# Optimization experiments

Hardware: AMD Instinct MI355X
Metric: run time of the kernel (lower is better)

The kernel has to match this reference:

```python
import jax, jax.numpy as jnp
import numpy as np

N = 50000      # atoms
E = 800000     # edges (flat neighbor list)
ELEM = 64      # elem_fea_len
NBR = 64       # nbr_fea_len
EPS = 1e-5


def _bn(x, gamma, beta):
    # BatchNorm1d in training mode: biased batch stats over dim 0
    mean = jnp.mean(x, axis=0)
    var = jnp.mean(jnp.square(x - mean), axis=0)
    return (x - mean) * jax.lax.rsqrt(var + EPS) * gamma + beta


def setup_inputs() -> dict:
    key = jax.random.key(0)
    ks = jax.random.split(key, 8)
    atom_in_fea = jax.random.normal(ks[0], (N, ELEM), dtype=jnp.float32)
    nbr_fea = jax.random.normal(ks[1], (E, NBR), dtype=jnp.float32)
    self_fea_idx = jnp.sort(jax.random.randint(ks[2], (E,), 0, N))
    nbr_fea_idx = jax.random.randint(ks[3], (E,), 0, N)
    d_in = 2 * ELEM + NBR
    d_out = 2 * ELEM
    W = jax.random.normal(ks[4], (d_in, d_out), dtype=jnp.float32) / np.sqrt(d_in)
    b = jax.random.normal(ks[5], (d_out,), dtype=jnp.float32) * 0.01
    bn1_gamma = jnp.ones((d_out,), jnp.float32)
    bn1_beta = jnp.zeros((d_out,), jnp.float32)
    bn2_gamma = jnp.ones((ELEM,), jnp.float32)
    bn2_beta = jnp.zeros((ELEM,), jnp.float32)
    return {
        "atom_in_fea": atom_in_fea, "nbr_fea": nbr_fea,
        "self_fea_idx": self_fea_idx, "nbr_fea_idx": nbr_fea_idx,
        "W": W, "b": b,
        "bn1_gamma": bn1_gamma, "bn1_beta": bn1_beta,
        "bn2_gamma": bn2_gamma, "bn2_beta": bn2_beta,
    }


def reference(atom_in_fea, nbr_fea, self_fea_idx, nbr_fea_idx,
              W, b, bn1_gamma, bn1_beta, bn2_gamma, bn2_beta):
    n_atoms = atom_in_fea.shape[0]
    # gather endpoint features: (E, ELEM) each
    atom_self = atom_in_fea[self_fea_idx]
    atom_nbr = atom_in_fea[nbr_fea_idx]
    total = jnp.concatenate([atom_self, atom_nbr, nbr_fea], axis=1)  # (E, 2*ELEM+NBR)
    total = total @ W + b                                            # (E, 2*ELEM)
    total = _bn(total, bn1_gamma, bn1_beta)
    filter_fea, core_fea = jnp.split(total, 2, axis=1)
    nbr_msg = jax.nn.sigmoid(filter_fea) * jax.nn.softplus(core_fea)  # (E, ELEM)
    nbr_sumed = jax.ops.segment_sum(nbr_msg, self_fea_idx, num_segments=n_atoms)
    nbr_sumed = _bn(nbr_sumed, bn2_gamma, bn2_beta)
    return jax.nn.softplus(atom_in_fea + nbr_sumed)
```

## Files before the change

kernel.cpp:

```cpp
#include <hip/hip_runtime.h>

typedef unsigned short ushort_t;
typedef __attribute__((ext_vector_type(8))) short short8;
typedef __attribute__((ext_vector_type(4))) float f32x4;

constexpr int N_ATOMS = 50000;
constexpr int N_EDGES = 800000;
constexpr int ELEM    = 64;
constexpr int D_IN    = 192;
constexpr int D_OUT   = 128;
constexpr float EPS   = 1e-5f;

constexpr int TILE_M = 64;
constexpr int NREP   = 16;

constexpr size_t OFF_NS   = 0;
constexpr size_t OFF_ABF  = OFF_NS   + (size_t)N_ATOMS * ELEM * 4;
constexpr size_t OFF_WT   = OFF_ABF  + (size_t)N_ATOMS * ELEM * 2;
constexpr size_t OFF_BN1  = OFF_WT   + (size_t)D_OUT * D_IN * 2;
constexpr size_t OFF_SC1  = OFF_BN1  + NREP * 256 * 4;
constexpr size_t OFF_BN2  = OFF_SC1  + 256 * 4;
constexpr size_t OFF_SC2  = OFF_BN2  + NREP * 128 * 4;

__device__ __forceinline__ ushort_t f32_to_bf16(float f) {
    unsigned int u = __float_as_uint(f);
    u = (u + 0x7fffu + ((u >> 16) & 1u)) >> 16;
    return (ushort_t)u;
}
__device__ __forceinline__ float bf16_to_f32(ushort_t h) {
    return __uint_as_float(((unsigned int)h) << 16);
}
__device__ __forceinline__ float softplus_f(float x) {
    return fmaxf(x, 0.f) + __logf(1.f + __expf(-fabsf(x)));
}

__global__ void prep_init_kernel(const float* __restrict__ atom, const float* __restrict__ W,
                                 ushort_t* __restrict__ abf, ushort_t* __restrict__ Wt,
                                 float* __restrict__ ns,
                                 float* __restrict__ bn1r, float* __restrict__ bn2r) {
    int i = blockIdx.x * blockDim.x + threadIdx.x;
    if (i < N_ATOMS * ELEM) { abf[i] = f32_to_bf16(atom[i]); ns[i] = 0.f; }
    if (i < D_IN * D_OUT) {
        int k = i >> 7, n = i & 127;
        Wt[n * D_IN + k] = f32_to_bf16(W[i]);
    }
    if (i < NREP * 256) bn1r[i] = 0.f;
    if (i < NREP * 128) bn2r[i] = 0.f;
}

__device__ __forceinline__ void stage_A(ushort_t (*As)[200],
                                        const ushort_t* __restrict__ abf,
                                        const float* __restrict__ nbrf,
                                        const int* __restrict__ sidx,
                                        const int* __restrict__ nidx,
                                        int e0, int tid) {
    #pragma unroll
    for (int ch = 0; ch < 2; ++ch) {
        const int* __restrict__ idx = ch ? nidx : sidx;
        #pragma unroll
        for (int i = 0; i < 2; ++i) {
            int r = (tid >> 3) + 32 * i;
            int h = tid & 7;
            const uint4* src = (const uint4*)(abf + (size_t)idx[e0 + r] * 64);
            *(uint4*)&As[r][ch * 64 + h * 8] = src[h];
        }
    }
    #pragma unroll
    for (int i = 0; i < 4; ++i) {
        int r  = (tid >> 4) + 16 * i;
        int c4 = tid & 15;
        float4 v = *(const float4*)(nbrf + (size_t)(e0 + r) * 64 + c4 * 4);
        ushort4 pk;
        pk.x = f32_to_bf16(v.x); pk.y = f32_to_bf16(v.y);
        pk.z = f32_to_bf16(v.z); pk.w = f32_to_bf16(v.w);
        *(ushort4*)&As[r][128 + c4 * 4] = pk;
    }
}

__global__ __launch_bounds__(256) void stats_kernel(
    const ushort_t* __restrict__ abf, const float* __restrict__ nbrf,
    const int* __restrict__ sidx, const int* __restrict__ nidx,
    const ushort_t* __restrict__ Wt, const float* __restrict__ bias,
    float* __restrict__ bn1r)
{
    __shared__ __align__(16) ushort_t As[64][200];
    const int tid = threadIdx.x;
    const int e0  = blockIdx.x * TILE_M;

    stage_A(As, abf, nbrf, sidx, nidx, e0, tid);

    const int wave = tid >> 6, lane = tid & 63;
    const int m16 = lane & 15, quad = lane >> 4;

    short8 bfrag[2][6];
    #pragma unroll
    for (int nt = 0; nt < 2; ++nt) {
        const ushort_t* bp = Wt + (size_t)(wave * 32 + nt * 16 + m16) * D_IN + quad * 8;
        #pragma unroll
        for (int ks = 0; ks < 6; ++ks) bfrag[nt][ks] = *(const short8*)(bp + ks * 32);
    }
    __syncthreads();

    f32x4 acc[4][2];
    #pragma unroll
    for (int mt = 0; mt < 4; ++mt)
        #pragma unroll
        for (int nt = 0; nt < 2; ++nt) acc[mt][nt] = (f32x4){0.f, 0.f, 0.f, 0.f};

    #pragma unroll
    for (int ks = 0; ks < 6; ++ks) {
        int ko = ks * 32 + quad * 8;
        #pragma unroll
        for (int mt = 0; mt < 4; ++mt) {
            short8 a = *(const short8*)&As[mt * 16 + m16][ko];
            acc[mt][0] = __builtin_amdgcn_mfma_f32_16x16x32_bf16(a, bfrag[0][ks], acc[mt][0], 0, 0, 0);
            acc[mt][1] = __builtin_amdgcn_mfma_f32_16x16x32_bf16(a, bfrag[1][ks], acc[mt][1], 0, 0, 0);
        }
    }

    float* rep = bn1r + (size_t)(blockIdx.x & (NREP - 1)) * 256;
    #pragma unroll
    for (int nt = 0; nt < 2; ++nt) {
        int c = wave * 32 + nt * 16 + m16;
        float b = bias[c];
        float s = 0.f, q = 0.f;
        #pragma unroll
        for (int mt = 0; mt < 4; ++mt)
            #pragma unroll
            for (int r = 0; r < 4; ++r) {
                float v = acc[mt][nt][r] + b;
                s += v; q += v * v;
            }
        s += __shfl_xor(s, 16); s += __shfl_xor(s, 32);
        q += __shfl_xor(q, 16); q += __shfl_xor(q, 32);
        if (quad == 0) {
            atomicAdd(&rep[c], s);
            atomicAdd(&rep[128 + c], q);
        }
    }
}

__global__ void bn1_finalize(const float* __restrict__ bn1r,
                             const float* __restrict__ g1, const float* __restrict__ b1,
                             float* __restrict__ sc) {
    int c = threadIdx.x;
    float s = 0.f, q = 0.f;
    #pragma unroll
    for (int r = 0; r < NREP; ++r) { s += bn1r[r * 256 + c]; q += bn1r[r * 256 + 128 + c]; }
    float mean = s * (1.f / N_EDGES);
    float var  = q * (1.f / N_EDGES) - mean * mean;
    float scale = g1[c] * rsqrtf(var + EPS);
    sc[c] = scale;
    sc[128 + c] = b1[c] - mean * scale;
}

__global__ __launch_bounds__(256) void msg_kernel(
    const ushort_t* __restrict__ abf, const float* __restrict__ nbrf,
    const int* __restrict__ sidx, const int* __restrict__ nidx,
    const ushort_t* __restrict__ Wt, const float* __restrict__ bias,
    const float* __restrict__ sc, float* __restrict__ ns)
{
    __shared__ __align__(16) char smem[25600];
    ushort_t (*As)[200] = (ushort_t(*)[200])smem;
    float    (*Ms)[68]  = (float(*)[68])smem;
    __shared__ int ss[64];

    const int tid = threadIdx.x;
    const int e0  = blockIdx.x * TILE_M;

    stage_A(As, abf, nbrf, sidx, nidx, e0, tid);
    if (tid < 64) ss[tid] = sidx[e0 + tid];

    const int wave = tid >> 6, lane = tid & 63;
    const int m16 = lane & 15, quad = lane >> 4;
    const int cf = wave * 16 + m16;
    const int cc = 64 + cf;

    short8 bfrag[2][6];
    {
        const ushort_t* bp0 = Wt + (size_t)cf * D_IN + quad * 8;
        const ushort_t* bp1 = Wt + (size_t)cc * D_IN + quad * 8;
        #pragma unroll
        for (int ks = 0; ks < 6; ++ks) {
            bfrag[0][ks] = *(const short8*)(bp0 + ks * 32);
            bfrag[1][ks] = *(const short8*)(bp1 + ks * 32);
        }
    }
    __syncthreads();

    f32x4 acc[4][2];
    #pragma unroll
    for (int mt = 0; mt < 4; ++mt)
        #pragma unroll
        for (int nt = 0; nt < 2; ++nt) acc[mt][nt] = (f32x4){0.f, 0.f, 0.f, 0.f};

    #pragma unroll
    for (int ks = 0; ks < 6; ++ks) {
        int ko = ks * 32 + quad * 8;
        #pragma unroll
        for (int mt = 0; mt < 4; ++mt) {
            short8 a = *(const short8*)&As[mt * 16 + m16][ko];
            acc[mt][0] = __builtin_amdgcn_mfma_f32_16x16x32_bf16(a, bfrag[0][ks], acc[mt][0], 0, 0, 0);
            acc[mt][1] = __builtin_amdgcn_mfma_f32_16x16x32_bf16(a, bfrag[1][ks], acc[mt][1], 0, 0, 0);
        }
    }
    __syncthreads();

    {
        float bf_ = bias[cf], bc_ = bias[cc];
        float scf = sc[cf], shf = sc[128 + cf];
        float scc = sc[cc], shc = sc[128 + cc];
        #pragma unroll
        for (int mt = 0; mt < 4; ++mt) {
            int row = mt * 16 + quad * 4;
            #pragma unroll
            for (int r = 0; r < 4; ++r) {
                float yf = fmaf(acc[mt][0][r] + bf_, scf, shf);
                float yc = fmaf(acc[mt][1][r] + bc_, scc, shc);
                Ms[row + r][cf] = softplus_f(yc) / (1.f + __expf(-yf));
            }
        }
    }
    __syncthreads();

    {
        int v = tid >> 6, c = tid & 63;
        int base = v * 16;
        int cur = ss[base];
        float a = 0.f;
        #pragma unroll
        for (int r = 0; r < 16; ++r) {
            int s = ss[base + r];
            if (s != cur) { atomicAdd(&ns[(size_t)cur * 64 + c], a); cur = s; a = 0.f; }
            a += Ms[base + r][c];
        }
        atomicAdd(&ns[(size_t)cur * 64 + c], a);
    }
}

__global__ __launch_bounds__(256) void bn2_stats_kernel(
    const float* __restrict__ ns, float* __restrict__ bn2r)
{
    int c = threadIdx.x & 63;
    float s = 0.f, q = 0.f;
    for (int a = blockIdx.x * 4 + (threadIdx.x >> 6); a < N_ATOMS; a += 4096) {
        float v = ns[a * ELEM + c];
        s += v; q += v * v;
    }
    float* rep = bn2r + (size_t)(blockIdx.x & (NREP - 1)) * 128;
    atomicAdd(&rep[c], s);
    atomicAdd(&rep[64 + c], q);
}

__global__ void bn2_finalize(const float* __restrict__ bn2r,
                             const float* __restrict__ g2, const float* __restrict__ b2,
                             float* __restrict__ sc2) {
    int c = threadIdx.x;
    float s = 0.f, q = 0.f;
    #pragma unroll
    for (int r = 0; r < NREP; ++r) { s += bn2r[r * 128 + c]; q += bn2r[r * 128 + 64 + c]; }
    float mean = s * (1.f / N_ATOMS);
    float var  = q * (1.f / N_ATOMS) - mean * mean;
    float scale = g2[c] * rsqrtf(var + EPS);
    sc2[c] = scale;
    sc2[64 + c] = b2[c] - mean * scale;
}

__global__ void final_kernel(const float* __restrict__ atom, const float* __restrict__ ns,
                             const float* __restrict__ sc2, float* __restrict__ out)
{
    int i = blockIdx.x * blockDim.x + threadIdx.x;
    if (i < N_ATOMS * ELEM) {
        int c = i & 63;
        float x = atom[i] + fmaf(ns[i], sc2[c], sc2[64 + c]);
        out[i] = softplus_f(x);
    }
}

extern "C" void kernel_launch(void* const* d_in, const int* in_sizes, int n_in,
                              void* d_out, int out_size, void* d_ws, size_t ws_size,
                              hipStream_t stream) {
    const float* atom = (const float*)d_in[0];
    const float* nbrf = (const float*)d_in[1];
    const int*   sidx = (const int*)d_in[2];
    const int*   nidx = (const int*)d_in[3];
    const float* W    = (const float*)d_in[4];
    const float* bias = (const float*)d_in[5];
    const float* g1   = (const float*)d_in[6];
    const float* b1   = (const float*)d_in[7];
    const float* g2   = (const float*)d_in[8];
    const float* b2   = (const float*)d_in[9];
    float* out = (float*)d_out;
    char*  ws  = (char*)d_ws;

    float*    ns   = (float*)(ws + OFF_NS);
    ushort_t* abf  = (ushort_t*)(ws + OFF_ABF);
    ushort_t* Wt   = (ushort_t*)(ws + OFF_WT);
    float*    bn1r = (float*)(ws + OFF_BN1);
    float*    sc1  = (float*)(ws + OFF_SC1);
    float*    bn2r = (float*)(ws + OFF_BN2);
    float*    sc2  = (float*)(ws + OFF_SC2);

    hipLaunchKernelGGL(prep_init_kernel, dim3((N_ATOMS * ELEM + 255) / 256), dim3(256), 0, stream,
                       atom, W, abf, Wt, ns, bn1r, bn2r);
    hipLaunchKernelGGL(stats_kernel, dim3(N_EDGES / TILE_M), dim3(256), 0, stream,
                       abf, nbrf, sidx, nidx, Wt, bias, bn1r);
    hipLaunchKernelGGL(bn1_finalize, dim3(1), dim3(128), 0, stream, bn1r, g1, b1, sc1);
    hipLaunchKernelGGL(msg_kernel, dim3(N_EDGES / TILE_M), dim3(256), 0, stream,
                       abf, nbrf, sidx, nidx, Wt, bias, sc1, ns);
    hipLaunchKernelGGL(bn2_stats_kernel, dim3(1024), dim3(256), 0, stream, ns, bn2r);
    hipLaunchKernelGGL(bn2_finalize, dim3(1), dim3(64), 0, stream, bn2r, g2, b2, sc2);
    hipLaunchKernelGGL(final_kernel, dim3((N_ATOMS * ELEM + 255) / 256), dim3(256), 0, stream,
                       atom, ns, sc2, out);
}
```

Measured before the change: 461.0 us.

## Cache bf16 edge features, fold BN finalize into consumers, split weight loads

The stats pass now reads nbr_fea with nontemporal loads and writes a bf16 copy to workspace, so the message pass reads half the bytes for edge features. The two BN finalize kernels are removed. Each consumer block recomputes the scale and shift from the replicated partial sums, and the linear bias is folded into the shift. Weight fragments are loaded in two halves to lower register pressure. In exchange the stats pass writes an extra 100MB and every block repeats the small finalize work.

```diff
diff --git a/kernel.cpp b/kernel.cpp
--- a/kernel.cpp
+++ b/kernel.cpp
@@ -3,6 +3,7 @@
 typedef unsigned short ushort_t;
 typedef __attribute__((ext_vector_type(8))) short short8;
 typedef __attribute__((ext_vector_type(4))) float f32x4;
+typedef __attribute__((ext_vector_type(4))) float vf4;
 
 constexpr int N_ATOMS = 50000;
 constexpr int N_EDGES = 800000;
@@ -16,19 +17,15 @@
 
 constexpr size_t OFF_NS   = 0;
 constexpr size_t OFF_ABF  = OFF_NS   + (size_t)N_ATOMS * ELEM * 4;
-constexpr size_t OFF_WT   = OFF_ABF  + (size_t)N_ATOMS * ELEM * 2;
+constexpr size_t OFF_NBF  = OFF_ABF  + (size_t)N_ATOMS * ELEM * 2;
+constexpr size_t OFF_WT   = OFF_NBF  + (size_t)N_EDGES * ELEM * 2;
 constexpr size_t OFF_BN1  = OFF_WT   + (size_t)D_OUT * D_IN * 2;
-constexpr size_t OFF_SC1  = OFF_BN1  + NREP * 256 * 4;
-constexpr size_t OFF_BN2  = OFF_SC1  + 256 * 4;
-constexpr size_t OFF_SC2  = OFF_BN2  + NREP * 128 * 4;
+constexpr size_t OFF_BN2  = OFF_BN1  + NREP * 256 * 4;
 
 __device__ __forceinline__ ushort_t f32_to_bf16(float f) {
     unsigned int u = __float_as_uint(f);
     u = (u + 0x7fffu + ((u >> 16) & 1u)) >> 16;
     return (ushort_t)u;
-}
-__device__ __forceinline__ float bf16_to_f32(ushort_t h) {
-    return __uint_as_float(((unsigned int)h) << 16);
 }
 __device__ __forceinline__ float softplus_f(float x) {
     return fmaxf(x, 0.f) + __logf(1.f + __expf(-fabsf(x)));
@@ -48,12 +45,11 @@
     if (i < NREP * 128) bn2r[i] = 0.f;
 }
 
-__device__ __forceinline__ void stage_A(ushort_t (*As)[200],
-                                        const ushort_t* __restrict__ abf,
-                                        const float* __restrict__ nbrf,
-                                        const int* __restrict__ sidx,
-                                        const int* __restrict__ nidx,
-                                        int e0, int tid) {
+__device__ __forceinline__ void stage_atoms(ushort_t (*As)[200],
+                                            const ushort_t* __restrict__ abf,
+                                            const int* __restrict__ sidx,
+                                            const int* __restrict__ nidx,
+                                            int e0, int tid) {
     #pragma unroll
     for (int ch = 0; ch < 2; ++ch) {
         const int* __restrict__ idx = ch ? nidx : sidx;
@@ -65,56 +61,62 @@
             *(uint4*)&As[r][ch * 64 + h * 8] = src[h];
         }
     }
+}
+
+__global__ __launch_bounds__(256) void stats_kernel(
+    const ushort_t* __restrict__ abf, const float* __restrict__ nbrf,
+    const int* __restrict__ sidx, const int* __restrict__ nidx,
+    const ushort_t* __restrict__ Wt, const float* __restrict__ bias,
+    ushort_t* __restrict__ nbrf_bf, float* __restrict__ bn1r)
+{
+    __shared__ __align__(16) ushort_t As[64][200];
+    const int tid = threadIdx.x;
+    const int e0  = blockIdx.x * TILE_M;
+
+    stage_atoms(As, abf, sidx, nidx, e0, tid);
     #pragma unroll
     for (int i = 0; i < 4; ++i) {
         int r  = (tid >> 4) + 16 * i;
         int c4 = tid & 15;
-        float4 v = *(const float4*)(nbrf + (size_t)(e0 + r) * 64 + c4 * 4);
+        vf4 v = __builtin_nontemporal_load((const vf4*)(nbrf + (size_t)(e0 + r) * 64 + c4 * 4));
         ushort4 pk;
         pk.x = f32_to_bf16(v.x); pk.y = f32_to_bf16(v.y);
         pk.z = f32_to_bf16(v.z); pk.w = f32_to_bf16(v.w);
         *(ushort4*)&As[r][128 + c4 * 4] = pk;
-    }
-}
-
-__global__ __launch_bounds__(256) void stats_kernel(
-    const ushort_t* __restrict__ abf, const float* __restrict__ nbrf,
-    const int* __restrict__ sidx, const int* __restrict__ nidx,
-    const ushort_t* __restrict__ Wt, const float* __restrict__ bias,
-    float* __restrict__ bn1r)
-{
-    __shared__ __align__(16) ushort_t As[64][200];
-    const int tid = threadIdx.x;
-    const int e0  = blockIdx.x * TILE_M;
-
-    stage_A(As, abf, nbrf, sidx, nidx, e0, tid);
+        *(ushort4*)&nbrf_bf[(size_t)(e0 + r) * 64 + c4 * 4] = pk;
+    }
 
     const int wave = tid >> 6, lane = tid & 63;
     const int m16 = lane & 15, quad = lane >> 4;
 
-    short8 bfrag[2][6];
-    #pragma unroll
-    for (int nt = 0; nt < 2; ++nt) {
-        const ushort_t* bp = Wt + (size_t)(wave * 32 + nt * 16 + m16) * D_IN + quad * 8;
-        #pragma unroll
-        for (int ks = 0; ks < 6; ++ks) bfrag[nt][ks] = *(const short8*)(bp + ks * 32);
-    }
-    __syncthreads();
-
     f32x4 acc[4][2];
     #pragma unroll
     for (int mt = 0; mt < 4; ++mt)
         #pragma unroll
         for (int nt = 0; nt < 2; ++nt) acc[mt][nt] = (f32x4){0.f, 0.f, 0.f, 0.f};
 
-    #pragma unroll
-    for (int ks = 0; ks < 6; ++ks) {
-        int ko = ks * 32 + quad * 8;
-        #pragma unroll
-        for (int mt = 0; mt < 4; ++mt) {
-            short8 a = *(const short8*)&As[mt * 16 + m16][ko];
-            acc[mt][0] = __builtin_amdgcn_mfma_f32_16x16x32_bf16(a, bfrag[0][ks], acc[mt][0], 0, 0, 0);
-            acc[mt][1] = __builtin_amdgcn_mfma_f32_16x16x32_bf16(a, bfrag[1][ks], acc[mt][1], 0, 0, 0);
+    const ushort_t* bp0 = Wt + (size_t)(wave * 32 + m16) * D_IN + quad * 8;
+    const ushort_t* bp1 = bp0 + 16 * D_IN;
+
+    __syncthreads();
+
+    #pragma unroll
+    for (int h = 0; h < 2; ++h) {
+        short8 b0[3], b1[3];
+        #pragma unroll
+        for (int ks = 0; ks < 3; ++ks) {
+            b0[ks] = *(const short8*)(bp0 + (h * 3 + ks) * 32);
+            b1[ks] = *(const short8*)(bp1 + (h * 3 + ks) * 32);
+        }
+        #pragma unroll
+        for (int ks = 0; ks < 3; ++ks) {
+            int ko = (h * 3 + ks) * 32 + quad * 8;
+            #pragma unroll
+            for (int mt = 0; mt < 4; ++mt) {
+                short8 a = *(const short8*)&As[mt * 16 + m16][ko];
+                acc[mt][0] = __builtin_amdgcn_mfma_f32_16x16x32_bf16(a, b0[ks], acc[mt][0], 0, 0, 0);
+                acc[mt][1] = __builtin_amdgcn_mfma_f32_16x16x32_bf16(a, b1[ks], acc[mt][1], 0, 0, 0);
+            }
         }
     }
 
@@ -140,35 +142,42 @@
     }
 }
 
-__global__ void bn1_finalize(const float* __restrict__ bn1r,
-                             const float* __restrict__ g1, const float* __restrict__ b1,
-                             float* __restrict__ sc) {
-    int c = threadIdx.x;
-    float s = 0.f, q = 0.f;
-    #pragma unroll
-    for (int r = 0; r < NREP; ++r) { s += bn1r[r * 256 + c]; q += bn1r[r * 256 + 128 + c]; }
-    float mean = s * (1.f / N_EDGES);
-    float var  = q * (1.f / N_EDGES) - mean * mean;
-    float scale = g1[c] * rsqrtf(var + EPS);
-    sc[c] = scale;
-    sc[128 + c] = b1[c] - mean * scale;
-}
-
 __global__ __launch_bounds__(256) void msg_kernel(
-    const ushort_t* __restrict__ abf, const float* __restrict__ nbrf,
+    const ushort_t* __restrict__ abf, const ushort_t* __restrict__ nbrf_bf,
     const int* __restrict__ sidx, const int* __restrict__ nidx,
     const ushort_t* __restrict__ Wt, const float* __restrict__ bias,
-    const float* __restrict__ sc, float* __restrict__ ns)
+    const float* __restrict__ bn1r, const float* __restrict__ g1,
+    const float* __restrict__ b1, float* __restrict__ ns)
 {
     __shared__ __align__(16) char smem[25600];
     ushort_t (*As)[200] = (ushort_t(*)[200])smem;
     float    (*Ms)[68]  = (float(*)[68])smem;
     __shared__ int ss[64];
+    __shared__ float scs[256];
 
     const int tid = threadIdx.x;
     const int e0  = blockIdx.x * TILE_M;
 
-    stage_A(As, abf, nbrf, sidx, nidx, e0, tid);
+    if (tid < 128) {
+        int c = tid;
+        float s = 0.f, q = 0.f;
+        #pragma unroll
+        for (int r = 0; r < NREP; ++r) { s += bn1r[r * 256 + c]; q += bn1r[r * 256 + 128 + c]; }
+        float mean = s * (1.f / N_EDGES);
+        float var  = q * (1.f / N_EDGES) - mean * mean;
+        float scale = g1[c] * rsqrtf(var + EPS);
+        scs[c] = scale;
+        scs[128 + c] = fmaf(bias[c] - mean, scale, b1[c]);
+    }
+
+    stage_atoms(As, abf, sidx, nidx, e0, tid);
+    #pragma unroll
+    for (int i = 0; i < 2; ++i) {
+        int r = (tid >> 3) + 32 * i;
+        int h = tid & 7;
+        const uint4* src = (const uint4*)(nbrf_bf + (size_t)(e0 + r) * 64);
+        *(uint4*)&As[r][128 + h * 8] = src[h];
+    }
     if (tid < 64) ss[tid] = sidx[e0 + tid];
 
     const int wave = tid >> 6, lane = tid & 63;
@@ -176,47 +185,48 @@
     const int cf = wave * 16 + m16;
     const int cc = 64 + cf;
 
-    short8 bfrag[2][6];
+    f32x4 acc[4][2];
+    #pragma unroll
+    for (int mt = 0; mt < 4; ++mt)
+        #pragma unroll
+        for (int nt = 0; nt < 2; ++nt) acc[mt][nt] = (f32x4){0.f, 0.f, 0.f, 0.f};
+
+    const ushort_t* bp0 = Wt + (size_t)cf * D_IN + quad * 8;
+    const ushort_t* bp1 = Wt + (size_t)cc * D_IN + quad * 8;
+
+    __syncthreads();
+
+    #pragma unroll
+    for (int h = 0; h < 2; ++h) {
+        short8 b0[3], b1v[3];
+        #pragma unroll
+        for (int ks = 0; ks < 3; ++ks) {
+            b0[ks]  = *(const short8*)(bp0 + (h * 3 + ks) * 32);
+            b1v[ks] = *(const short8*)(bp1 + (h * 3 + ks) * 32);
+        }
+        #pragma unroll
+        for (int ks = 0; ks < 3; ++ks) {
+            int ko = (h * 3 + ks) * 32 + quad * 8;
+            #pragma unroll
+            for (int mt = 0; mt < 4; ++mt) {
+                short8 a = *(const short8*)&As[mt * 16 + m16][ko];
+                acc[mt][0] = __builtin_amdgcn_mfma_f32_16x16x32_bf16(a, b0[ks], acc[mt][0], 0, 0, 0);
+                acc[mt][1] = __builtin_amdgcn_mfma_f32_16x16x32_bf16(a, b1v[ks], acc[mt][1], 0, 0, 0);
+            }
+        }
+    }
+    __syncthreads();
+
     {
-        const ushort_t* bp0 = Wt + (size_t)cf * D_IN + quad * 8;
-        const ushort_t* bp1 = Wt + (size_t)cc * D_IN + quad * 8;
-        #pragma unroll
-        for (int ks = 0; ks < 6; ++ks) {
-            bfrag[0][ks] = *(const short8*)(bp0 + ks * 32);
-            bfrag[1][ks] = *(const short8*)(bp1 + ks * 32);
-        }
-    }
-    __syncthreads();
-
-    f32x4 acc[4][2];
-    #pragma unroll
-    for (int mt = 0; mt < 4; ++mt)
-        #pragma unroll
-        for (int nt = 0; nt < 2; ++nt) acc[mt][nt] = (f32x4){0.f, 0.f, 0.f, 0.f};
-
-    #pragma unroll
-    for (int ks = 0; ks < 6; ++ks) {
-        int ko = ks * 32 + quad * 8;
-        #pragma unroll
-        for (int mt = 0; mt < 4; ++mt) {
-            short8 a = *(const short8*)&As[mt * 16 + m16][ko];
-            acc[mt][0] = __builtin_amdgcn_mfma_f32_16x16x32_bf16(a, bfrag[0][ks], acc[mt][0], 0, 0, 0);
-            acc[mt][1] = __builtin_amdgcn_mfma_f32_16x16x32_bf16(a, bfrag[1][ks], acc[mt][1], 0, 0, 0);
-        }
-    }
-    __syncthreads();
-
-    {
-        float bf_ = bias[cf], bc_ = bias[cc];
-        float scf = sc[cf], shf = sc[128 + cf];
-        float scc = sc[cc], shc = sc[128 + cc];
+        float scf = scs[cf], shf = scs[128 + cf];
+        float scc = scs[cc], shc = scs[128 + cc];
         #pragma unroll
         for (int mt = 0; mt < 4; ++mt) {
             int row = mt * 16 + quad * 4;
             #pragma unroll
             for (int r = 0; r < 4; ++r) {
-                float yf = fmaf(acc[mt][0][r] + bf_, scf, shf);
-                float yc = fmaf(acc[mt][1][r] + bc_, scc, shc);
+                float yf = fmaf(acc[mt][0][r], scf, shf);
+                float yc = fmaf(acc[mt][1][r], scc, shc);
                 Ms[row + r][cf] = softplus_f(yc) / (1.f + __expf(-yf));
             }
         }
@@ -252,27 +262,28 @@
     atomicAdd(&rep[64 + c], q);
 }
 
-__global__ void bn2_finalize(const float* __restrict__ bn2r,
-                             const float* __restrict__ g2, const float* __restrict__ b2,
-                             float* __restrict__ sc2) {
-    int c = threadIdx.x;
-    float s = 0.f, q = 0.f;
-    #pragma unroll
-    for (int r = 0; r < NREP; ++r) { s += bn2r[r * 128 + c]; q += bn2r[r * 128 + 64 + c]; }
-    float mean = s * (1.f / N_ATOMS);
-    float var  = q * (1.f / N_ATOMS) - mean * mean;
-    float scale = g2[c] * rsqrtf(var + EPS);
-    sc2[c] = scale;
-    sc2[64 + c] = b2[c] - mean * scale;
-}
-
-__global__ void final_kernel(const float* __restrict__ atom, const float* __restrict__ ns,
-                             const float* __restrict__ sc2, float* __restrict__ out)
+__global__ __launch_bounds__(256) void final_kernel(
+    const float* __restrict__ atom, const float* __restrict__ ns,
+    const float* __restrict__ bn2r, const float* __restrict__ g2,
+    const float* __restrict__ b2, float* __restrict__ out)
 {
-    int i = blockIdx.x * blockDim.x + threadIdx.x;
+    __shared__ float sc2s[128];
+    int t = threadIdx.x;
+    if (t < 64) {
+        float s = 0.f, q = 0.f;
+        #pragma unroll
+        for (int r = 0; r < NREP; ++r) { s += bn2r[r * 128 + t]; q += bn2r[r * 128 + 64 + t]; }
+        float mean = s * (1.f / N_ATOMS);
+        float var  = q * (1.f / N_ATOMS) - mean * mean;
+        float scale = g2[t] * rsqrtf(var + EPS);
+        sc2s[t] = scale;
+        sc2s[64 + t] = b2[t] - mean * scale;
+    }
+    __syncthreads();
+    int i = blockIdx.x * 256 + t;
     if (i < N_ATOMS * ELEM) {
-        int c = i & 63;
-        float x = atom[i] + fmaf(ns[i], sc2[c], sc2[64 + c]);
+        int c = t & 63;
+        float x = atom[i] + fmaf(ns[i], sc2s[c], sc2s[64 + c]);
         out[i] = softplus_f(x);
     }
 }
@@ -293,23 +304,20 @@
     float* out = (float*)d_out;
     char*  ws  = (char*)d_ws;
 
-    float*    ns   = (float*)(ws + OFF_NS);
-    ushort_t* abf  = (ushort_t*)(ws + OFF_ABF);
-    ushort_t* Wt   = (ushort_t*)(ws + OFF_WT);
-    float*    bn1r = (float*)(ws + OFF_BN1);
-    float*    sc1  = (float*)(ws + OFF_SC1);
-    float*    bn2r = (float*)(ws + OFF_BN2);
-    float*    sc2  = (float*)(ws + OFF_SC2);
+    float*    ns    = (float*)(ws + OFF_NS);
+    ushort_t* abf   = (ushort_t*)(ws + OFF_ABF);
+    ushort_t* nbf   = (ushort_t*)(ws + OFF_NBF);
+    ushort_t* Wt    = (ushort_t*)(ws + OFF_WT);
+    float*    bn1r  = (float*)(ws + OFF_BN1);
+    float*    bn2r  = (float*)(ws + OFF_BN2);
 
     hipLaunchKernelGGL(prep_init_kernel, dim3((N_ATOMS * ELEM + 255) / 256), dim3(256), 0, stream,
                        atom, W, abf, Wt, ns, bn1r, bn2r);
     hipLaunchKernelGGL(stats_kernel, dim3(N_EDGES / TILE_M), dim3(256), 0, stream,
-                       abf, nbrf, sidx, nidx, Wt, bias, bn1r);
-    hipLaunchKernelGGL(bn1_finalize, dim3(1), dim3(128), 0, stream, bn1r, g1, b1, sc1);
+                       abf, nbrf, sidx, nidx, Wt, bias, nbf, bn1r);
     hipLaunchKernelGGL(msg_kernel, dim3(N_EDGES / TILE_M), dim3(256), 0, stream,
-                       abf, nbrf, sidx, nidx, Wt, bias, sc1, ns);
+                       abf, nbf, sidx, nidx, Wt, bias, bn1r, g1, b1, ns);
     hipLaunchKernelGGL(bn2_stats_kernel, dim3(1024), dim3(256), 0, stream, ns, bn2r);
-    hipLaunchKernelGGL(bn2_finalize, dim3(1), dim3(64), 0, stream, bn2r, g2, b2, sc2);
     hipLaunchKernelGGL(final_kernel, dim3((N_ATOMS * ELEM + 255) / 256), dim3(256), 0, stream,
-                       atom, ns, sc2, out);
-}
+                       atom, ns, bn2r, g2, b2, out);
+}
```

Result: slower. 498.4 us (+8.1%).
